# Kernel optimization log

Measured on AMD Instinct MI355X. Metric: run time of the kernel, lower is better.

The kernel has to match this reference:

```python
import jax, jax.numpy as jnp
import numpy as np

B, L, D, H = 2, 2048, 2048, 16
Dh = D // H
THETA = 500000.0


def _init_rope(dim, seq_len, n_heads):
    # Returns freqs_cis of shape (1, seq_len, 1, head_dim//2, 2) -> [..., 0]=cos, [..., 1]=sin
    hd = dim // n_heads
    inv_freqs = 1.0 / (THETA ** (jnp.arange(0, hd, 2, dtype=jnp.float32) / hd))
    t = jnp.arange(seq_len, dtype=jnp.float32)
    freqs = jnp.outer(t, inv_freqs).astype(jnp.float32)  # (L, hd/2)
    fc = jnp.stack([jnp.cos(freqs)[None, :, None, :],
                    jnp.sin(freqs)[None, :, None, :]], axis=3)  # (1, L, 1, 2, hd/2)
    return fc.transpose(0, 1, 2, 4, 3)  # (1, L, 1, hd/2, 2)


def _apply_rope(q, k, freqs_cis):
    def rotate(x):
        x2 = x.reshape(*x.shape[:-1], -1, 2)  # (B, L, H, Dh/2, 2)
        f = freqs_cis[:, :x.shape[1]]
        cos, sin = f[..., 0], f[..., 1]
        r = jnp.stack([x2[..., 0] * cos - x2[..., 1] * sin,
                       x2[..., 1] * cos + x2[..., 0] * sin], axis=-1)
        return r.reshape(*x.shape)
    return rotate(q), rotate(k)


def setup_inputs() -> dict:
    key = jax.random.key(0)
    kx, kq, kk, kv, ko = jax.random.split(key, 5)
    scale = 1.0 / np.sqrt(D)
    x = jax.random.normal(kx, (B, L, D), dtype=jnp.float32)
    Wq = jax.random.normal(kq, (D, H, Dh), dtype=jnp.float32) * scale
    Wk = jax.random.normal(kk, (D, H, Dh), dtype=jnp.float32) * scale
    Wv = jax.random.normal(kv, (D, H, Dh), dtype=jnp.float32) * scale
    Wo = jax.random.normal(ko, (D, D), dtype=jnp.float32) * scale
    return {"x": x, "Wq": Wq, "Wk": Wk, "Wv": Wv, "Wo": Wo}


def reference(x, Wq, Wk, Wv, Wo):
    freqs_cis = _init_rope(D, L, H)
    q = jnp.einsum('bld,dhk->blhk', x, Wq)  # (B, L, H, Dh)
    k = jnp.einsum('bld,dhk->blhk', x, Wk)
    v = jnp.einsum('bld,dhk->blhk', x, Wv)
    q, k = _apply_rope(q, k, freqs_cis)
    q = q / (Dh ** 0.5)
    att = jnp.einsum('bqhd,bkhd->bhqk', q, k)  # (B, H, L, L)
    Lq = x.shape[1]
    mask = jnp.tril(jnp.ones((1, 1, Lq, Lq), dtype=jnp.bool_))
    neg_inf = jnp.finfo(jnp.float32).min
    att = jnp.where(mask, att, neg_inf)
    att = jax.nn.softmax(att, axis=-1)
    out = jnp.einsum('bhqk,bkhd->bqhd', att, v)  # (B, L, H, Dh)
    out = out.reshape(x.shape)
    return jnp.einsum('bld,de->ble', out, Wo)
```

## Files before the change

kernel.cpp:

```cpp
#include <hip/hip_runtime.h>

typedef unsigned short u16;
typedef unsigned int u32;

#define Bb 2
#define Lc 2048
#define Dc 2048
#define Hc 16
#define DhC 128

typedef __bf16 bf16x8 __attribute__((ext_vector_type(8)));
typedef float f32x4 __attribute__((ext_vector_type(4)));

__device__ __forceinline__ u16 f2b(float f) {
  u32 u = __float_as_uint(f);
  u32 r = (u + 0x7fffu + ((u >> 16) & 1u)) >> 16;
  return (u16)r;
}
__device__ __forceinline__ float b2f(u16 u) {
  return __uint_as_float(((u32)u) << 16);
}

__device__ __forceinline__ void gll16(const void* g, void* l) {
  __builtin_amdgcn_global_load_lds(
      (const __attribute__((address_space(1))) u32*)g,
      (__attribute__((address_space(3))) u32*)l, 16, 0, 0);
}

__global__ __launch_bounds__(256) void sniff_dtype(const u16* __restrict__ x,
                                                   int* __restrict__ flag) {
  __shared__ int bad;
  if (threadIdx.x == 0) bad = 0;
  __syncthreads();
  int local = 0;
  for (int i = threadIdx.x; i < 65536; i += 256) {
    float v = fabsf(b2f(x[i]));
    if (!(v < 1000.f)) local = 1;
  }
  if (local) atomicOr(&bad, 1);
  __syncthreads();
  if (threadIdx.x == 0) *flag = bad;
}

__global__ __launch_bounds__(256) void conv_x(const void* __restrict__ in,
                                              u16* __restrict__ out,
                                              const int* __restrict__ flag) {
  const int f32 = *flag;
  const int i0 = (blockIdx.x * 256 + threadIdx.x) * 4;
  if (f32) {
    const float* p = (const float*)in;
#pragma unroll
    for (int j = 0; j < 4; j++) out[i0 + j] = f2b(p[i0 + j]);
  } else {
    const u16* p = (const u16*)in;
#pragma unroll
    for (int j = 0; j < 4; j++) out[i0 + j] = p[i0 + j];
  }
}

__global__ __launch_bounds__(256) void transpose2d_conv(const void* __restrict__ in,
                                                        u16* __restrict__ out,
                                                        const int* __restrict__ flag) {
  __shared__ __align__(16) u16 tile[64][65];
  const int f32 = *flag;
  const int r0 = blockIdx.y * 64, c0 = blockIdx.x * 64;
  const int tc = threadIdx.x & 63, tr4 = threadIdx.x >> 6;
#pragma unroll
  for (int p = 0; p < 16; p++) {
    int r = tr4 + p * 4;
    size_t idx = (size_t)(r0 + r) * 2048 + c0 + tc;
    tile[r][tc] = f32 ? f2b(((const float*)in)[idx]) : ((const u16*)in)[idx];
  }
  __syncthreads();
#pragma unroll
  for (int p = 0; p < 16; p++) {
    int rr = tr4 + p * 4;
    out[(size_t)(c0 + rr) * 2048 + r0 + tc] = tile[tc][rr];
  }
}

template <typename OutT>
__device__ __forceinline__ void gemm_bt_core(const u16* __restrict__ A,
                                             const u16* __restrict__ Bt,
                                             OutT* __restrict__ C) {
  constexpr int K = 2048, N = 2048;
  __shared__ __align__(16) u16 As[128 * 64];
  __shared__ __align__(16) u16 Bs[128 * 64];
  const int tid = threadIdx.x;
  const int lane = tid & 63, wid = tid >> 6;
  const int wm = (wid >> 1) * 64, wn = (wid & 1) * 64;
  const int m0 = blockIdx.x * 128, n0 = blockIdx.y * 128;
  const int quad = lane >> 4, l15 = lane & 15;
  const int sw = l15 & 7;

  const f32x4 fz = {0.f, 0.f, 0.f, 0.f};
  f32x4 acc[4][4];
#pragma unroll
  for (int i = 0; i < 4; i++)
#pragma unroll
    for (int j = 0; j < 4; j++) acc[i][j] = fz;

  const int srl = (lane >> 3);
  const int ssl = lane & 7;

  for (int k0 = 0; k0 < K; k0 += 64) {
#pragma unroll
    for (int p = 0; p < 4; p++) {
      const int r = p * 32 + wid * 8 + srl;
      const int c = ssl ^ (r & 7);
      u16* lb = As + (p * 256 + wid * 64) * 8;
      gll16(A + (size_t)(m0 + r) * K + k0 + c * 8, lb);
    }
#pragma unroll
    for (int p = 0; p < 4; p++) {
      const int r = p * 32 + wid * 8 + srl;
      const int c = ssl ^ (r & 7);
      u16* lb = Bs + (p * 256 + wid * 64) * 8;
      gll16(Bt + (size_t)(n0 + r) * K + k0 + c * 8, lb);
    }
    __syncthreads();
#pragma unroll
    for (int ks = 0; ks < 2; ks++) {
      bf16x8 af[4], bfr[4];
#pragma unroll
      for (int t = 0; t < 4; t++) {
        const int cc = ((ks * 4 + quad) ^ sw) * 8;
        af[t]  = *(const bf16x8*)(&As[(wm + t * 16 + l15) * 64 + cc]);
        bfr[t] = *(const bf16x8*)(&Bs[(wn + t * 16 + l15) * 64 + cc]);
      }
#pragma unroll
      for (int mt = 0; mt < 4; mt++)
#pragma unroll
        for (int nt = 0; nt < 4; nt++)
          acc[mt][nt] = __builtin_amdgcn_mfma_f32_16x16x32_bf16(af[mt], bfr[nt], acc[mt][nt], 0, 0, 0);
    }
    __syncthreads();
  }
#pragma unroll
  for (int mt = 0; mt < 4; mt++)
#pragma unroll
    for (int nt = 0; nt < 4; nt++) {
      int col = n0 + wn + nt * 16 + l15;
#pragma unroll
      for (int r = 0; r < 4; r++) {
        int row = m0 + wm + mt * 16 + quad * 4 + r;
        float v = acc[mt][nt][r];
        if constexpr (sizeof(OutT) == 2)
          C[(size_t)row * N + col] = f2b(v);
        else
          C[(size_t)row * N + col] = v;
      }
    }
}

__global__ __launch_bounds__(256) void gemm_bt(const u16* __restrict__ A,
                                               const u16* __restrict__ Bt,
                                               u16* __restrict__ C) {
  gemm_bt_core<u16>(A, Bt, C);
}
__global__ __launch_bounds__(256) void gemm_bt_f32(const u16* __restrict__ A,
                                                   const u16* __restrict__ Bt,
                                                   float* __restrict__ C) {
  gemm_bt_core<float>(A, Bt, C);
}

__global__ __launch_bounds__(256) void transpose_v_k(const u16* __restrict__ V,
                                                     u16* __restrict__ Vt) {
  __shared__ __align__(16) u16 tile[64][65];
  const int z = blockIdx.z;
  const int b = z >> 4, h = z & 15;
  const int l0 = blockIdx.y * 64, d0 = blockIdx.x * 64;
  const int tc = threadIdx.x & 63, tr4 = threadIdx.x >> 6;
#pragma unroll
  for (int p = 0; p < 16; p++) {
    int l = tr4 + p * 4;
    tile[l][tc] = V[(size_t)((b * Lc + l0 + l) * Hc + h) * DhC + d0 + tc];
  }
  __syncthreads();
#pragma unroll
  for (int p = 0; p < 16; p++) {
    int dd = tr4 + p * 4;
    Vt[((size_t)z * DhC + d0 + dd) * Lc + l0 + tc] = tile[tc][dd];
  }
}

__global__ __launch_bounds__(256) void rope_qk(u16* __restrict__ Q, u16* __restrict__ K) {
  const int idx = blockIdx.x * 256 + threadIdx.x;
  const int j = idx & 63;
  const int l = (idx >> 10) & 2047;
  const float inv = expf(-0.2050369278f * (float)j);
  const float ang = (float)l * inv;
  float s, c;
  sincosf(ang, &s, &c);
  const size_t off = (size_t)idx * 2;
  const float q0 = b2f(Q[off]), q1 = b2f(Q[off + 1]);
  const float k0 = b2f(K[off]), k1 = b2f(K[off + 1]);
  const float sc = 0.08838834764f;
  Q[off]     = f2b((q0 * c - q1 * s) * sc);
  Q[off + 1] = f2b((q1 * c + q0 * s) * sc);
  K[off]     = f2b(k0 * c - k1 * s);
  K[off + 1] = f2b(k1 * c + k0 * s);
}

#define NEGBIG (-3.0e30f)
__global__ __launch_bounds__(256) void flash_attn(const u16* __restrict__ Q,
                                                  const u16* __restrict__ Kg,
                                                  const u16* __restrict__ Vt,
                                                  u16* __restrict__ O) {
  __shared__ __align__(16) u16 Ks[2][64 * 128];
  __shared__ __align__(16) u16 Vs[2][128 * 64];
  __shared__ __align__(16) u16 Ps[4][16][72];
  const int tid = threadIdx.x;
  const int lane = tid & 63, w = tid >> 6;
  const int quad = lane >> 4, l15 = lane & 15;
  const int qt = (int)gridDim.x - 1 - (int)blockIdx.x;
  const int bh = blockIdx.y;
  const int b = bh >> 4, h = bh & 15;
  const int q0 = qt * 64;
  const int qrow = q0 + w * 16 + l15;

  const int krl = lane >> 4, ksl = lane & 15;
  const int vrl = lane >> 3, vsl = lane & 7;

  bf16x8 aq[4];
  const u16* qptr = Q + ((size_t)(b * Lc + qrow) * Hc + h) * DhC + quad * 8;
#pragma unroll
  for (int ks = 0; ks < 4; ks++) aq[ks] = *(const bf16x8*)(qptr + ks * 32);

  {
#pragma unroll
    for (int p = 0; p < 4; p++) {
      const int r = p * 16 + w * 4 + krl;
      const int c = ksl ^ (r & 15);
      gll16(Kg + ((size_t)(b * Lc + r) * Hc + h) * DhC + c * 8,
            &Ks[0][(p * 256 + w * 64) * 8]);
    }
#pragma unroll
    for (int p = 0; p < 4; p++) {
      const int r = p * 32 + w * 8 + vrl;
      const int c = vsl ^ (r & 7);
      gll16(Vt + ((size_t)bh * DhC + r) * Lc + c * 8,
            &Vs[0][(p * 256 + w * 64) * 8]);
    }
  }

  const f32x4 fz = {0.f, 0.f, 0.f, 0.f};
  f32x4 o[8];
#pragma unroll
  for (int f = 0; f < 8; f++) o[f] = fz;
  float mrow[4], lrow[4];
#pragma unroll
  for (int r = 0; r < 4; r++) { mrow[r] = NEGBIG; lrow[r] = 0.f; }

  __syncthreads();

  for (int kvt = 0; kvt <= qt; kvt++) {
    const int cur = kvt & 1;
    const u16* Ksc = Ks[cur];
    const u16* Vsc = Vs[cur];

    if (kvt < qt) {
      const int nv0 = (kvt + 1) * 64;
      const int nxt = cur ^ 1;
#pragma unroll
      for (int p = 0; p < 4; p++) {
        const int r = p * 16 + w * 4 + krl;
        const int c = ksl ^ (r & 15);
        gll16(Kg + ((size_t)(b * Lc + nv0 + r) * Hc + h) * DhC + c * 8,
              &Ks[nxt][(p * 256 + w * 64) * 8]);
      }
#pragma unroll
      for (int p = 0; p < 4; p++) {
        const int r = p * 32 + w * 8 + vrl;
        const int c = vsl ^ (r & 7);
        gll16(Vt + ((size_t)bh * DhC + r) * Lc + nv0 + c * 8,
              &Vs[nxt][(p * 256 + w * 64) * 8]);
      }
    }

    f32x4 s[4];
#pragma unroll
    for (int ct = 0; ct < 4; ct++) s[ct] = fz;
#pragma unroll
    for (int ks = 0; ks < 4; ks++) {
#pragma unroll
      for (int ct = 0; ct < 4; ct++) {
        bf16x8 bk = *(const bf16x8*)(
            &Ksc[(ct * 16 + l15) * 128 + (((ks << 2) + quad) ^ l15) * 8]);
        s[ct] = __builtin_amdgcn_mfma_f32_16x16x32_bf16(aq[ks], bk, s[ct], 0, 0, 0);
      }
    }

    if (kvt == qt) {
      const int kv0 = kvt * 64;
#pragma unroll
      for (int ct = 0; ct < 4; ct++) {
        int kvc = kv0 + ct * 16 + l15;
#pragma unroll
        for (int r = 0; r < 4; r++) {
          int qr = q0 + w * 16 + quad * 4 + r;
          if (kvc > qr) s[ct][r] = NEGBIG;
        }
      }
    }

    float mnew[4], alpha[4];
#pragma unroll
    for (int r = 0; r < 4; r++) {
      float mx = fmaxf(fmaxf(s[0][r], s[1][r]), fmaxf(s[2][r], s[3][r]));
#pragma unroll
      for (int off = 1; off < 16; off <<= 1) mx = fmaxf(mx, __shfl_xor(mx, off, 64));
      mnew[r] = fmaxf(mrow[r], mx);
      alpha[r] = __expf(mrow[r] - mnew[r]);
      mrow[r] = mnew[r];
    }
    float psum[4] = {0.f, 0.f, 0.f, 0.f};
#pragma unroll
    for (int ct = 0; ct < 4; ct++) {
#pragma unroll
      for (int r = 0; r < 4; r++) {
        float p = __expf(s[ct][r] - mnew[r]);
        s[ct][r] = p;
        psum[r] += p;
      }
    }
#pragma unroll
    for (int r = 0; r < 4; r++) {
#pragma unroll
      for (int off = 1; off < 16; off <<= 1) psum[r] += __shfl_xor(psum[r], off, 64);
      lrow[r] = lrow[r] * alpha[r] + psum[r];
    }
#pragma unroll
    for (int f = 0; f < 8; f++)
#pragma unroll
      for (int r = 0; r < 4; r++) o[f][r] *= alpha[r];

#pragma unroll
    for (int ct = 0; ct < 4; ct++)
#pragma unroll
      for (int r = 0; r < 4; r++)
        Ps[w][quad * 4 + r][ct * 16 + l15] = f2b(s[ct][r]);

#pragma unroll
    for (int ks = 0; ks < 2; ks++) {
      bf16x8 ap = *(const bf16x8*)(&Ps[w][l15][ks * 32 + quad * 8]);
#pragma unroll
      for (int f = 0; f < 8; f++) {
        bf16x8 bv = *(const bf16x8*)(
            &Vsc[(f * 16 + l15) * 64 + ((((ks << 2) + quad)) ^ (l15 & 7)) * 8]);
        o[f] = __builtin_amdgcn_mfma_f32_16x16x32_bf16(ap, bv, o[f], 0, 0, 0);
      }
    }

    __syncthreads();
  }

#pragma unroll
  for (int f = 0; f < 8; f++) {
    int d = f * 16 + l15;
#pragma unroll
    for (int r = 0; r < 4; r++) {
      int qr = q0 + w * 16 + quad * 4 + r;
      O[((size_t)(b * Lc + qr) * Hc + h) * DhC + d] = f2b(o[f][r] / lrow[r]);
    }
  }
}

extern "C" void kernel_launch(void* const* d_in, const int* in_sizes, int n_in,
                              void* d_out, int out_size, void* d_ws, size_t ws_size,
                              hipStream_t stream) {
  const void* x  = d_in[0];
  const void* Wq = d_in[1];
  const void* Wk = d_in[2];
  const void* Wv = d_in[3];
  const void* Wo = d_in[4];
  float* out = (float*)d_out;

  char* w = (char*)d_ws;
  const size_t WSZ = (size_t)2048 * 2048;
  const size_t XSZ = (size_t)Bb * Lc * Dc;
  int* flag = (int*)w;
  u16* WT  = (u16*)(w + 256);
  u16* xc  = WT + WSZ;
  u16* Qb  = xc + XSZ;
  u16* Kb  = Qb + XSZ;
  u16* Vb  = Kb + XSZ;
  u16* Vtb = xc;
  u16* Ob  = Vb;

  sniff_dtype<<<1, 256, 0, stream>>>((const u16*)x, flag);
  conv_x<<<(int)(XSZ / 1024), 256, 0, stream>>>(x, xc, flag);

  dim3 tgrid(32, 32);
  dim3 ggrid(32, 16);

  transpose2d_conv<<<tgrid, 256, 0, stream>>>(Wq, WT, flag);
  gemm_bt<<<ggrid, 256, 0, stream>>>(xc, WT, Qb);
  transpose2d_conv<<<tgrid, 256, 0, stream>>>(Wk, WT, flag);
  gemm_bt<<<ggrid, 256, 0, stream>>>(xc, WT, Kb);
  transpose2d_conv<<<tgrid, 256, 0, stream>>>(Wv, WT, flag);
  gemm_bt<<<ggrid, 256, 0, stream>>>(xc, WT, Vb);

  rope_qk<<<(Bb * Lc * Hc * 64) / 256, 256, 0, stream>>>(Qb, Kb);

  dim3 vgrid(2, 32, 32);
  transpose_v_k<<<vgrid, 256, 0, stream>>>(Vb, Vtb);

  dim3 fgrid(32, 32);
  flash_attn<<<fgrid, 256, 0, stream>>>(Qb, Kb, Vtb, Ob);

  transpose2d_conv<<<tgrid, 256, 0, stream>>>(Wo, WT, flag);
  gemm_bt_f32<<<ggrid, 256, 0, stream>>>(Ob, WT, out);
}
```

Baseline: 586.8 us.

## Fuse QKV GEMMs, shrink attention KV tile, use exp2 and MFMA row sums

```diff
diff --git a/kernel.cpp b/kernel.cpp
--- a/kernel.cpp
+++ b/kernel.cpp
@@ -79,44 +79,29 @@
   }
 }
 
-template <typename OutT>
-__device__ __forceinline__ void gemm_bt_core(const u16* __restrict__ A,
-                                             const u16* __restrict__ Bt,
-                                             OutT* __restrict__ C) {
-  constexpr int K = 2048, N = 2048;
-  __shared__ __align__(16) u16 As[128 * 64];
-  __shared__ __align__(16) u16 Bs[128 * 64];
+__device__ __forceinline__ void gemm_kloop(const u16* __restrict__ A, int m0,
+                                           const u16* __restrict__ BtB,
+                                           u16* As, u16* Bs, f32x4 (*acc)[4]) {
+  constexpr int K = 2048;
   const int tid = threadIdx.x;
   const int lane = tid & 63, wid = tid >> 6;
   const int wm = (wid >> 1) * 64, wn = (wid & 1) * 64;
-  const int m0 = blockIdx.x * 128, n0 = blockIdx.y * 128;
   const int quad = lane >> 4, l15 = lane & 15;
   const int sw = l15 & 7;
-
-  const f32x4 fz = {0.f, 0.f, 0.f, 0.f};
-  f32x4 acc[4][4];
-#pragma unroll
-  for (int i = 0; i < 4; i++)
-#pragma unroll
-    for (int j = 0; j < 4; j++) acc[i][j] = fz;
-
-  const int srl = (lane >> 3);
-  const int ssl = lane & 7;
+  const int srl = (lane >> 3), ssl = lane & 7;
 
   for (int k0 = 0; k0 < K; k0 += 64) {
 #pragma unroll
     for (int p = 0; p < 4; p++) {
       const int r = p * 32 + wid * 8 + srl;
       const int c = ssl ^ (r & 7);
-      u16* lb = As + (p * 256 + wid * 64) * 8;
-      gll16(A + (size_t)(m0 + r) * K + k0 + c * 8, lb);
+      gll16(A + (size_t)(m0 + r) * K + k0 + c * 8, As + (p * 256 + wid * 64) * 8);
     }
 #pragma unroll
     for (int p = 0; p < 4; p++) {
       const int r = p * 32 + wid * 8 + srl;
       const int c = ssl ^ (r & 7);
-      u16* lb = Bs + (p * 256 + wid * 64) * 8;
-      gll16(Bt + (size_t)(n0 + r) * K + k0 + c * 8, lb);
+      gll16(BtB + (size_t)r * K + k0 + c * 8, Bs + (p * 256 + wid * 64) * 8);
     }
     __syncthreads();
 #pragma unroll
@@ -136,6 +121,32 @@
     }
     __syncthreads();
   }
+}
+
+__global__ __launch_bounds__(256) void gemm_qkv(const u16* __restrict__ A,
+                                                const u16* __restrict__ WTall,
+                                                u16* __restrict__ Qo,
+                                                u16* __restrict__ Ko,
+                                                u16* __restrict__ Vo) {
+  __shared__ __align__(16) u16 As[128 * 64];
+  __shared__ __align__(16) u16 Bs[128 * 64];
+  const int m0 = blockIdx.x * 128;
+  const int n0g = blockIdx.y * 128;
+  u16* Co = (n0g < 2048) ? Qo : (n0g < 4096) ? Ko : Vo;
+  const int n0 = n0g & 2047;
+
+  const f32x4 fz = {0.f, 0.f, 0.f, 0.f};
+  f32x4 acc[4][4];
+#pragma unroll
+  for (int i = 0; i < 4; i++)
+#pragma unroll
+    for (int j = 0; j < 4; j++) acc[i][j] = fz;
+
+  gemm_kloop(A, m0, WTall + (size_t)n0g * 2048, As, Bs, acc);
+
+  const int lane = threadIdx.x & 63, wid = threadIdx.x >> 6;
+  const int wm = (wid >> 1) * 64, wn = (wid & 1) * 64;
+  const int quad = lane >> 4, l15 = lane & 15;
 #pragma unroll
   for (int mt = 0; mt < 4; mt++)
 #pragma unroll
@@ -144,24 +155,41 @@
 #pragma unroll
       for (int r = 0; r < 4; r++) {
         int row = m0 + wm + mt * 16 + quad * 4 + r;
-        float v = acc[mt][nt][r];
-        if constexpr (sizeof(OutT) == 2)
-          C[(size_t)row * N + col] = f2b(v);
-        else
-          C[(size_t)row * N + col] = v;
+        Co[(size_t)row * 2048 + col] = f2b(acc[mt][nt][r]);
       }
     }
 }
 
-__global__ __launch_bounds__(256) void gemm_bt(const u16* __restrict__ A,
-                                               const u16* __restrict__ Bt,
-                                               u16* __restrict__ C) {
-  gemm_bt_core<u16>(A, Bt, C);
-}
 __global__ __launch_bounds__(256) void gemm_bt_f32(const u16* __restrict__ A,
                                                    const u16* __restrict__ Bt,
                                                    float* __restrict__ C) {
-  gemm_bt_core<float>(A, Bt, C);
+  __shared__ __align__(16) u16 As[128 * 64];
+  __shared__ __align__(16) u16 Bs[128 * 64];
+  const int m0 = blockIdx.x * 128, n0 = blockIdx.y * 128;
+
+  const f32x4 fz = {0.f, 0.f, 0.f, 0.f};
+  f32x4 acc[4][4];
+#pragma unroll
+  for (int i = 0; i < 4; i++)
+#pragma unroll
+    for (int j = 0; j < 4; j++) acc[i][j] = fz;
+
+  gemm_kloop(A, m0, Bt + (size_t)n0 * 2048, As, Bs, acc);
+
+  const int lane = threadIdx.x & 63, wid = threadIdx.x >> 6;
+  const int wm = (wid >> 1) * 64, wn = (wid & 1) * 64;
+  const int quad = lane >> 4, l15 = lane & 15;
+#pragma unroll
+  for (int mt = 0; mt < 4; mt++)
+#pragma unroll
+    for (int nt = 0; nt < 4; nt++) {
+      int col = n0 + wn + nt * 16 + l15;
+#pragma unroll
+      for (int r = 0; r < 4; r++) {
+        int row = m0 + wm + mt * 16 + quad * 4 + r;
+        C[(size_t)row * 2048 + col] = acc[mt][nt][r];
+      }
+    }
 }
 
 __global__ __launch_bounds__(256) void transpose_v_k(const u16* __restrict__ V,
@@ -195,7 +223,7 @@
   const size_t off = (size_t)idx * 2;
   const float q0 = b2f(Q[off]), q1 = b2f(Q[off + 1]);
   const float k0 = b2f(K[off]), k1 = b2f(K[off + 1]);
-  const float sc = 0.08838834764f;
+  const float sc = 0.1275187487f;
   Q[off]     = f2b((q0 * c - q1 * s) * sc);
   Q[off + 1] = f2b((q1 * c + q0 * s) * sc);
   K[off]     = f2b(k0 * c - k1 * s);
@@ -207,9 +235,9 @@
                                                   const u16* __restrict__ Kg,
                                                   const u16* __restrict__ Vt,
                                                   u16* __restrict__ O) {
-  __shared__ __align__(16) u16 Ks[2][64 * 128];
-  __shared__ __align__(16) u16 Vs[2][128 * 64];
-  __shared__ __align__(16) u16 Ps[4][16][72];
+  __shared__ __align__(16) u16 Ks[2][32 * 128];
+  __shared__ __align__(16) u16 Vs[2][128 * 32];
+  __shared__ __align__(16) u16 Ps[4][16][40];
   const int tid = threadIdx.x;
   const int lane = tid & 63, w = tid >> 6;
   const int quad = lane >> 4, l15 = lane & 15;
@@ -219,82 +247,67 @@
   const int q0 = qt * 64;
   const int qrow = q0 + w * 16 + l15;
 
-  const int krl = lane >> 4, ksl = lane & 15;
-  const int vrl = lane >> 3, vsl = lane & 7;
-
   bf16x8 aq[4];
   const u16* qptr = Q + ((size_t)(b * Lc + qrow) * Hc + h) * DhC + quad * 8;
 #pragma unroll
   for (int ks = 0; ks < 4; ks++) aq[ks] = *(const bf16x8*)(qptr + ks * 32);
 
-  {
-#pragma unroll
-    for (int p = 0; p < 4; p++) {
-      const int r = p * 16 + w * 4 + krl;
-      const int c = ksl ^ (r & 15);
-      gll16(Kg + ((size_t)(b * Lc + r) * Hc + h) * DhC + c * 8,
-            &Ks[0][(p * 256 + w * 64) * 8]);
-    }
-#pragma unroll
-    for (int p = 0; p < 4; p++) {
-      const int r = p * 32 + w * 8 + vrl;
-      const int c = vsl ^ (r & 7);
-      gll16(Vt + ((size_t)bh * DhC + r) * Lc + c * 8,
-            &Vs[0][(p * 256 + w * 64) * 8]);
-    }
-  }
+  bf16x8 one8;
+#pragma unroll
+  for (int j = 0; j < 8; j++) one8[j] = (__bf16)1.0f;
+
+  const int k_r = w * 4 + (lane >> 4);
+  const int k_gc = (lane & 15) ^ k_r;
+  const int v_r = w * 16 + (lane >> 2);
+  const int v_gc = (lane & 3) ^ (lane >> 4);
+
+#define STAGE_KV(kv0, buf)                                                        \
+  {                                                                               \
+    _Pragma("unroll") for (int p = 0; p < 2; p++)                                 \
+        gll16(Kg + ((size_t)(b * Lc + (kv0) + p * 16 + k_r) * Hc + h) * DhC +     \
+                  k_gc * 8,                                                       \
+              &Ks[buf][(p * 256 + w * 64) * 8]);                                  \
+    _Pragma("unroll") for (int p = 0; p < 2; p++)                                 \
+        gll16(Vt + ((size_t)bh * DhC + p * 64 + v_r) * Lc + (kv0) + v_gc * 8,     \
+              &Vs[buf][(p * 256 + w * 64) * 8]);                                  \
+  }
+
+  STAGE_KV(0, 0);
 
   const f32x4 fz = {0.f, 0.f, 0.f, 0.f};
   f32x4 o[8];
 #pragma unroll
   for (int f = 0; f < 8; f++) o[f] = fz;
-  float mrow[4], lrow[4];
-#pragma unroll
-  for (int r = 0; r < 4; r++) { mrow[r] = NEGBIG; lrow[r] = 0.f; }
+  f32x4 psacc = fz;
+  float mrow[4];
+#pragma unroll
+  for (int r = 0; r < 4; r++) mrow[r] = NEGBIG;
 
   __syncthreads();
 
-  for (int kvt = 0; kvt <= qt; kvt++) {
+  const int ntiles = 2 * qt + 2;
+  for (int kvt = 0; kvt < ntiles; kvt++) {
     const int cur = kvt & 1;
     const u16* Ksc = Ks[cur];
     const u16* Vsc = Vs[cur];
 
-    if (kvt < qt) {
-      const int nv0 = (kvt + 1) * 64;
-      const int nxt = cur ^ 1;
-#pragma unroll
-      for (int p = 0; p < 4; p++) {
-        const int r = p * 16 + w * 4 + krl;
-        const int c = ksl ^ (r & 15);
-        gll16(Kg + ((size_t)(b * Lc + nv0 + r) * Hc + h) * DhC + c * 8,
-              &Ks[nxt][(p * 256 + w * 64) * 8]);
-      }
-#pragma unroll
-      for (int p = 0; p < 4; p++) {
-        const int r = p * 32 + w * 8 + vrl;
-        const int c = vsl ^ (r & 7);
-        gll16(Vt + ((size_t)bh * DhC + r) * Lc + nv0 + c * 8,
-              &Vs[nxt][(p * 256 + w * 64) * 8]);
-      }
-    }
-
-    f32x4 s[4];
-#pragma unroll
-    for (int ct = 0; ct < 4; ct++) s[ct] = fz;
+    if (kvt + 1 < ntiles) STAGE_KV((kvt + 1) * 32, cur ^ 1);
+
+    f32x4 s[2] = {fz, fz};
 #pragma unroll
     for (int ks = 0; ks < 4; ks++) {
 #pragma unroll
-      for (int ct = 0; ct < 4; ct++) {
+      for (int ct = 0; ct < 2; ct++) {
         bf16x8 bk = *(const bf16x8*)(
             &Ksc[(ct * 16 + l15) * 128 + (((ks << 2) + quad) ^ l15) * 8]);
         s[ct] = __builtin_amdgcn_mfma_f32_16x16x32_bf16(aq[ks], bk, s[ct], 0, 0, 0);
       }
     }
 
-    if (kvt == qt) {
-      const int kv0 = kvt * 64;
-#pragma unroll
-      for (int ct = 0; ct < 4; ct++) {
+    if (kvt >= 2 * qt) {
+      const int kv0 = kvt * 32;
+#pragma unroll
+      for (int ct = 0; ct < 2; ct++) {
         int kvc = kv0 + ct * 16 + l15;
 #pragma unroll
         for (int r = 0; r < 4; r++) {
@@ -307,50 +320,38 @@
     float mnew[4], alpha[4];
 #pragma unroll
     for (int r = 0; r < 4; r++) {
-      float mx = fmaxf(fmaxf(s[0][r], s[1][r]), fmaxf(s[2][r], s[3][r]));
+      float mx = fmaxf(s[0][r], s[1][r]);
 #pragma unroll
       for (int off = 1; off < 16; off <<= 1) mx = fmaxf(mx, __shfl_xor(mx, off, 64));
       mnew[r] = fmaxf(mrow[r], mx);
-      alpha[r] = __expf(mrow[r] - mnew[r]);
+      alpha[r] = exp2f(mrow[r] - mnew[r]);
       mrow[r] = mnew[r];
     }
-    float psum[4] = {0.f, 0.f, 0.f, 0.f};
-#pragma unroll
-    for (int ct = 0; ct < 4; ct++) {
-#pragma unroll
-      for (int r = 0; r < 4; r++) {
-        float p = __expf(s[ct][r] - mnew[r]);
-        s[ct][r] = p;
-        psum[r] += p;
-      }
-    }
-#pragma unroll
-    for (int r = 0; r < 4; r++) {
-#pragma unroll
-      for (int off = 1; off < 16; off <<= 1) psum[r] += __shfl_xor(psum[r], off, 64);
-      lrow[r] = lrow[r] * alpha[r] + psum[r];
-    }
+#pragma unroll
+    for (int ct = 0; ct < 2; ct++)
+#pragma unroll
+      for (int r = 0; r < 4; r++) s[ct][r] = exp2f(s[ct][r] - mnew[r]);
 #pragma unroll
     for (int f = 0; f < 8; f++)
 #pragma unroll
       for (int r = 0; r < 4; r++) o[f][r] *= alpha[r];
-
-#pragma unroll
-    for (int ct = 0; ct < 4; ct++)
+#pragma unroll
+    for (int r = 0; r < 4; r++) psacc[r] *= alpha[r];
+
+#pragma unroll
+    for (int ct = 0; ct < 2; ct++)
 #pragma unroll
       for (int r = 0; r < 4; r++)
         Ps[w][quad * 4 + r][ct * 16 + l15] = f2b(s[ct][r]);
-
-#pragma unroll
-    for (int ks = 0; ks < 2; ks++) {
-      bf16x8 ap = *(const bf16x8*)(&Ps[w][l15][ks * 32 + quad * 8]);
-#pragma unroll
-      for (int f = 0; f < 8; f++) {
-        bf16x8 bv = *(const bf16x8*)(
-            &Vsc[(f * 16 + l15) * 64 + ((((ks << 2) + quad)) ^ (l15 & 7)) * 8]);
-        o[f] = __builtin_amdgcn_mfma_f32_16x16x32_bf16(ap, bv, o[f], 0, 0, 0);
-      }
-    }
+    bf16x8 ap = *(const bf16x8*)(&Ps[w][l15][quad * 8]);
+
+#pragma unroll
+    for (int f = 0; f < 8; f++) {
+      bf16x8 bv = *(const bf16x8*)(
+          &Vsc[(f * 16 + l15) * 32 + (quad ^ ((l15 >> 2) & 3)) * 8]);
+      o[f] = __builtin_amdgcn_mfma_f32_16x16x32_bf16(ap, bv, o[f], 0, 0, 0);
+    }
+    psacc = __builtin_amdgcn_mfma_f32_16x16x32_bf16(ap, one8, psacc, 0, 0, 0);
 
     __syncthreads();
   }
@@ -361,7 +362,7 @@
 #pragma unroll
     for (int r = 0; r < 4; r++) {
       int qr = q0 + w * 16 + quad * 4 + r;
-      O[((size_t)(b * Lc + qr) * Hc + h) * DhC + d] = f2b(o[f][r] / lrow[r]);
+      O[((size_t)(b * Lc + qr) * Hc + h) * DhC + d] = f2b(o[f][r] / psacc[r]);
     }
   }
 }
@@ -380,8 +381,9 @@
   const size_t WSZ = (size_t)2048 * 2048;
   const size_t XSZ = (size_t)Bb * Lc * Dc;
   int* flag = (int*)w;
-  u16* WT  = (u16*)(w + 256);
-  u16* xc  = WT + WSZ;
+  u16* WTall = (u16*)(w + 256);
+  u16* WoT = WTall + 3 * WSZ;
+  u16* xc  = WoT + WSZ;
   u16* Qb  = xc + XSZ;
   u16* Kb  = Qb + XSZ;
   u16* Vb  = Kb + XSZ;
@@ -392,14 +394,13 @@
   conv_x<<<(int)(XSZ / 1024), 256, 0, stream>>>(x, xc, flag);
 
   dim3 tgrid(32, 32);
-  dim3 ggrid(32, 16);
-
-  transpose2d_conv<<<tgrid, 256, 0, stream>>>(Wq, WT, flag);
-  gemm_bt<<<ggrid, 256, 0, stream>>>(xc, WT, Qb);
-  transpose2d_conv<<<tgrid, 256, 0, stream>>>(Wk, WT, flag);
-  gemm_bt<<<ggrid, 256, 0, stream>>>(xc, WT, Kb);
-  transpose2d_conv<<<tgrid, 256, 0, stream>>>(Wv, WT, flag);
-  gemm_bt<<<ggrid, 256, 0, stream>>>(xc, WT, Vb);
+  transpose2d_conv<<<tgrid, 256, 0, stream>>>(Wq, WTall, flag);
+  transpose2d_conv<<<tgrid, 256, 0, stream>>>(Wk, WTall + WSZ, flag);
+  transpose2d_conv<<<tgrid, 256, 0, stream>>>(Wv, WTall + 2 * WSZ, flag);
+  transpose2d_conv<<<tgrid, 256, 0, stream>>>(Wo, WoT, flag);
+
+  dim3 qkvgrid(32, 48);
+  gemm_qkv<<<qkvgrid, 256, 0, stream>>>(xc, WTall, Qb, Kb, Vb);
 
   rope_qk<<<(Bb * Lc * Hc * 64) / 256, 256, 0, stream>>>(Qb, Kb);
 
@@ -409,6 +410,6 @@
   dim3 fgrid(32, 32);
   flash_attn<<<fgrid, 256, 0, stream>>>(Qb, Kb, Vtb, Ob);
 
-  transpose2d_conv<<<tgrid, 256, 0, stream>>>(Wo, WT, flag);
-  gemm_bt_f32<<<ggrid, 256, 0, stream>>>(Ob, WT, out);
-}
+  dim3 ogrid(32, 16);
+  gemm_bt_f32<<<ogrid, 256, 0, stream>>>(Ob, WoT, out);
+}
```

After: 614.5 us. +4.7%, slower.
